# Kernel optimization log

Measured on AMD Instinct MI355X. Metric: run time of the kernel, lower is better.

Reference implementation:

```python
import jax, jax.numpy as jnp
import numpy as np

S = 16          # slice count (init kwarg)
EPS = 1e-5      # BN2d default eps


def markov_sub(m, s):
    """Vectorized get_markov_sub. m: [C, C] -> [s, C, C].
    ms[i][a,b] = where(m[i,b] > 0, m[a,b], 0); mss[k] = max over rows i in slice k.
    Equivalent closed form via per-column any/all positivity of the slice rows."""
    C = m.shape[0]
    pos = (m > 0.0).reshape(s, C // s, C)          # [s, slice_size, C]
    any_p = pos.any(axis=1)[:, None, :]            # [s, 1, C]
    all_p = pos.all(axis=1)[:, None, :]            # [s, 1, C]
    mb = m[None, :, :]                             # [1, C, C]
    return jnp.where(all_p, mb,
                     jnp.where(any_p, jnp.maximum(mb, 0.0), jnp.zeros_like(mb)))


def setup_inputs() -> dict:
    key = jax.random.key(0)
    ks = jax.random.split(key, 8)
    N, C, H, W = 4, 256, 32, 32
    s = S
    feats = jax.random.normal(ks[0], (N, C, H, W), jnp.float32)
    adj_matrix = jax.random.normal(ks[1], (N, C, C), jnp.float32)
    # three 1x1 conv layers: in = S*C, out = C (stacked on leading axis)
    conv_w = jax.random.normal(ks[2], (3, C, s * C), jnp.float32) / np.sqrt(s * C).astype(np.float32)
    conv_b = jax.random.normal(ks[3], (3, C), jnp.float32) * 0.01
    bn_gamma = jnp.ones((3, C), jnp.float32)
    bn_beta = jnp.zeros((3, C), jnp.float32)
    bn_mean = jax.random.normal(ks[4], (3, C), jnp.float32) * 0.1
    bn_var = jax.random.uniform(ks[5], (3, C), jnp.float32, minval=0.5, maxval=1.5)
    return {"feats": feats, "adj_matrix": adj_matrix, "conv_w": conv_w,
            "conv_b": conv_b, "bn_gamma": bn_gamma, "bn_beta": bn_beta,
            "bn_mean": bn_mean, "bn_var": bn_var}


def reference(feats, adj_matrix, conv_w, conv_b, bn_gamma, bn_beta, bn_mean, bn_var):
    N, C, H, W = feats.shape
    s = S
    # per-sample markov sub-adjacencies, computed once and reused across layers
    mss = jax.vmap(lambda m: markov_sub(m, s))(adj_matrix)      # [N, S, C, C]
    mss = mss.reshape(N, s * C, C)                              # [N, S*C, C]
    outs = []
    x = feats
    for l in range(3):
        xp = x.reshape(N, C, H * W)                             # [N, C, HW]
        y = jnp.einsum('nkc,ncp->nkp', mss, xp)                 # sparse.mm -> [N, S*C, HW]
        y = jnp.einsum('ok,nkp->nop', conv_w[l], y) + conv_b[l][None, :, None]
        scale = (bn_gamma[l] * jax.lax.rsqrt(bn_var[l] + EPS))[None, :, None]
        y = (y - bn_mean[l][None, :, None]) * scale + bn_beta[l][None, :, None]
        y = jax.nn.relu(y).reshape(N, C, H, W)
        outs.append(y)
        x = y
    return tuple(outs)
```

## Files before the change

kernel.cpp:

```cpp
#include <hip/hip_runtime.h>
#include <stdint.h>

#define CC   256
#define SSL  16
#define NB   4
#define HWP  1024
#define K1   4096
#define EPSV 1e-5f

typedef __attribute__((ext_vector_type(8))) short bf16x8;
typedef __attribute__((ext_vector_type(4))) float f32x4;

__device__ __forceinline__ ushort f2bf(float f) {
    uint32_t u = __float_as_uint(f);
    uint32_t r = (u + 0x7FFFu + ((u >> 16) & 1u)) >> 16;
    return (ushort)r;
}

__global__ __launch_bounds__(256) void flags_kernel(const float* __restrict__ adj,
                                                    uint8_t* __restrict__ flags) {
    const int nk = blockIdx.x;
    const int n = nk >> 4, k = nk & 15;
    const int b = threadIdx.x;
    const float* m = adj + (size_t)n * CC * CC;
    bool allp = true, anyp = false;
#pragma unroll
    for (int i = 0; i < 16; ++i) {
        float v = m[(size_t)(k * 16 + i) * CC + b];
        bool p = v > 0.0f;
        allp = allp && p;
        anyp = anyp || p;
    }
    flags[(size_t)nk * CC + b] = allp ? (uint8_t)2 : (anyp ? (uint8_t)1 : (uint8_t)0);
}

__global__ __launch_bounds__(256) void convw_bf16_kernel(const float* __restrict__ w,
                                                         ushort* __restrict__ wb) {
    const int idx = (blockIdx.x * 256 + threadIdx.x) * 4;
    float4 v = *(const float4*)(w + idx);
    ushort4 o = {f2bf(v.x), f2bf(v.y), f2bf(v.z), f2bf(v.w)};
    *(ushort4*)(wb + idx) = o;
}

__global__ __launch_bounds__(256) void msst_kernel(const float* __restrict__ adj,
                                                   const uint8_t* __restrict__ flags,
                                                   ushort* __restrict__ msst) {
    const int n = blockIdx.y;
    const int at = blockIdx.x >> 2, bt = blockIdx.x & 3;
    const int a0 = at * 64, b0 = bt * 64;
    const float* m = adj + (size_t)n * CC * CC;
    __shared__ float Ms[64][68];
    __shared__ uint8_t Fl[16][64];
    const int t = threadIdx.x;
    {
        const int ar = t >> 2, bq = (t & 3) * 16;
        const float* src = m + (size_t)(a0 + ar) * CC + b0 + bq;
#pragma unroll
        for (int i = 0; i < 4; ++i)
            *(float4*)&Ms[ar][bq + i * 4] = *(const float4*)(src + i * 4);
        const int k = t >> 4, b4 = (t & 15) * 4;
        *(uchar4*)&Fl[k][b4] = *(const uchar4*)(flags + (size_t)(n * SSL + k) * CC + b0 + b4);
    }
    __syncthreads();
    const int bl = t >> 2, ac = (t & 3) * 16;
    ushort bx[16], bp[16];
#pragma unroll
    for (int i = 0; i < 16; ++i) {
        float x = Ms[ac + i][bl];
        bx[i] = f2bf(x);
        bp[i] = f2bf(fmaxf(x, 0.0f));
    }
    ushort* dst = msst + ((size_t)(n * CC + b0 + bl)) * K1 + a0 + ac;
#pragma unroll
    for (int k = 0; k < 16; ++k) {
        const uint8_t f = Fl[k][bl];
        ushort* dk = dst + k * CC;
#pragma unroll
        for (int a4 = 0; a4 < 4; ++a4) {
            ushort4 o;
            o.x = (f == 2) ? bx[a4 * 4 + 0] : ((f == 1) ? bp[a4 * 4 + 0] : (ushort)0);
            o.y = (f == 2) ? bx[a4 * 4 + 1] : ((f == 1) ? bp[a4 * 4 + 1] : (ushort)0);
            o.z = (f == 2) ? bx[a4 * 4 + 2] : ((f == 1) ? bp[a4 * 4 + 2] : (ushort)0);
            o.w = (f == 2) ? bx[a4 * 4 + 3] : ((f == 1) ? bp[a4 * 4 + 3] : (ushort)0);
            *(ushort4*)(dk + a4 * 4) = o;
        }
    }
}

__global__ __launch_bounds__(256) void featsT_kernel(const float* __restrict__ feats,
                                                     ushort* __restrict__ fT) {
    const int n = blockIdx.y;
    const int ct = blockIdx.x >> 4, pt = blockIdx.x & 15;
    const int c0 = ct * 64, p0 = pt * 64;
    const float* src = feats + ((size_t)n * CC + c0) * HWP + p0;
    __shared__ float Ts[64][68];
    const int t = threadIdx.x;
    const int cr = t >> 2, pq = (t & 3) * 16;
#pragma unroll
    for (int i = 0; i < 4; ++i)
        *(float4*)&Ts[cr][pq + i * 4] = *(const float4*)(src + (size_t)cr * HWP + pq + i * 4);
    __syncthreads();
    const int pl = t >> 2, cc0 = (t & 3) * 16;
    ushort* dst = fT + ((size_t)n * HWP + p0 + pl) * CC + c0 + cc0;
#pragma unroll
    for (int a4 = 0; a4 < 4; ++a4) {
        ushort4 o;
        o.x = f2bf(Ts[cc0 + a4 * 4 + 0][pl]);
        o.y = f2bf(Ts[cc0 + a4 * 4 + 1][pl]);
        o.z = f2bf(Ts[cc0 + a4 * 4 + 2][pl]);
        o.w = f2bf(Ts[cc0 + a4 * 4 + 3][pl]);
        *(ushort4*)(dst + a4 * 4) = o;
    }
}

__global__ __launch_bounds__(256) void weff_mfma(const ushort* __restrict__ Aw,
                                                 const ushort* __restrict__ Bm,
                                                 float* __restrict__ wpart) {
    const int tile = blockIdx.x;
    const int ln = blockIdx.y;
    const int sp = blockIdx.z;
    const int l = ln >> 2, n = ln & 3;
    const int trow = (tile >> 1) * 128, tcol = (tile & 1) * 128;
    const ushort* A = Aw + (size_t)l * CC * K1;
    const ushort* B = Bm + (size_t)n * CC * K1;
    __shared__ ushort Al[128][40];
    __shared__ ushort Bl[128][40];
    const int t = threadIdx.x;
    const int wv = t >> 6, L = t & 63;
    const int wr = (wv >> 1) * 64, wc = (wv & 1) * 64;
    const int l16 = L & 15, q = L >> 4;
    const int r0 = t >> 2, kq0 = (t & 3) * 8;
    f32x4 acc[4][4];
#pragma unroll
    for (int i = 0; i < 4; ++i)
#pragma unroll
        for (int j = 0; j < 4; ++j)
            acc[i][j] = (f32x4){0.f, 0.f, 0.f, 0.f};

    const int kbase = sp * 512;
    for (int kt = 0; kt < 16; ++kt) {
        const int kk = kbase + kt * 32;
        int4 a0 = *(const int4*)(A + (size_t)(trow + r0) * K1 + kk + kq0);
        int4 a1 = *(const int4*)(A + (size_t)(trow + 64 + r0) * K1 + kk + kq0);
        int4 b0 = *(const int4*)(B + (size_t)(tcol + r0) * K1 + kk + kq0);
        int4 b1 = *(const int4*)(B + (size_t)(tcol + 64 + r0) * K1 + kk + kq0);
        __syncthreads();
        *(int4*)&Al[r0][kq0] = a0;
        *(int4*)&Al[64 + r0][kq0] = a1;
        *(int4*)&Bl[r0][kq0] = b0;
        *(int4*)&Bl[64 + r0][kq0] = b1;
        __syncthreads();
        bf16x8 af[4], bfr[4];
#pragma unroll
        for (int i = 0; i < 4; ++i)
            af[i] = *(const bf16x8*)&Al[wr + i * 16 + l16][q * 8];
#pragma unroll
        for (int j = 0; j < 4; ++j)
            bfr[j] = *(const bf16x8*)&Bl[wc + j * 16 + l16][q * 8];
#pragma unroll
        for (int i = 0; i < 4; ++i)
#pragma unroll
            for (int j = 0; j < 4; ++j)
                acc[i][j] = __builtin_amdgcn_mfma_f32_16x16x32_bf16(af[i], bfr[j], acc[i][j], 0, 0, 0);
    }

    float* W = wpart + ((size_t)sp * 12 + ln) * (CC * CC);
#pragma unroll
    for (int i = 0; i < 4; ++i)
#pragma unroll
        for (int j = 0; j < 4; ++j) {
            const int o = trow + wr + i * 16 + q * 4;
            const int b = tcol + wc + j * 16 + l16;
#pragma unroll
            for (int r = 0; r < 4; ++r)
                W[(size_t)(o + r) * CC + b] = acc[i][j][r];
        }
}

__global__ __launch_bounds__(256) void reduce_kernel(const float* __restrict__ wpart,
                                                     const float* __restrict__ gamma,
                                                     const float* __restrict__ var,
                                                     ushort* __restrict__ Ws) {
    const int idx = (blockIdx.x * 256 + threadIdx.x) * 4;
    const int ln = idx >> 16;
    const int l = ln >> 2;
    const int o = (idx >> 8) & 255;
    float4 s = {0.f, 0.f, 0.f, 0.f};
#pragma unroll
    for (int sp = 0; sp < 8; ++sp) {
        float4 v = *(const float4*)(wpart + (size_t)sp * 12 * 65536 + idx);
        s.x += v.x; s.y += v.y; s.z += v.z; s.w += v.w;
    }
    const float sc = gamma[l * CC + o] * rsqrtf(var[l * CC + o] + EPSV);
    ushort4 ob = {f2bf(s.x * sc), f2bf(s.y * sc), f2bf(s.z * sc), f2bf(s.w * sc)};
    *(ushort4*)(Ws + idx) = ob;
}

__global__ __launch_bounds__(256) void layer_mfma(const ushort* __restrict__ xT,
                                                  const ushort* __restrict__ Wsl,
                                                  const float* __restrict__ convb_l,
                                                  const float* __restrict__ gamma_l,
                                                  const float* __restrict__ beta_l,
                                                  const float* __restrict__ mean_l,
                                                  const float* __restrict__ var_l,
                                                  float* __restrict__ outl,
                                                  ushort* __restrict__ xTn) {
    const int n = blockIdx.y;
    const int pt = blockIdx.x & 15, ot = blockIdx.x >> 4;
    const ushort* Axt = xT + (size_t)n * HWP * CC + (size_t)pt * 64 * CC;
    const ushort* Bw  = Wsl + (size_t)n * CC * CC + (size_t)ot * 64 * CC;
    __shared__ ushort Al[64][40];
    __shared__ ushort Bl[64][40];
    const int t = threadIdx.x;
    const int wv = t >> 6, L = t & 63;
    const int wr = (wv >> 1) * 32, wc = (wv & 1) * 32;
    const int l16 = L & 15, q = L >> 4;
    const int r0 = t >> 2, kq0 = (t & 3) * 8;
    f32x4 acc[2][2];
#pragma unroll
    for (int i = 0; i < 2; ++i)
#pragma unroll
        for (int j = 0; j < 2; ++j)
            acc[i][j] = (f32x4){0.f, 0.f, 0.f, 0.f};

    for (int kt = 0; kt < 8; ++kt) {
        const int kk = kt * 32;
        int4 av = *(const int4*)(Axt + (size_t)r0 * CC + kk + kq0);
        int4 bv = *(const int4*)(Bw + (size_t)r0 * CC + kk + kq0);
        __syncthreads();
        *(int4*)&Al[r0][kq0] = av;
        *(int4*)&Bl[r0][kq0] = bv;
        __syncthreads();
        bf16x8 af[2], bfr[2];
#pragma unroll
        for (int i = 0; i < 2; ++i)
            af[i] = *(const bf16x8*)&Al[wr + i * 16 + l16][q * 8];
#pragma unroll
        for (int j = 0; j < 2; ++j)
            bfr[j] = *(const bf16x8*)&Bl[wc + j * 16 + l16][q * 8];
#pragma unroll
        for (int i = 0; i < 2; ++i)
#pragma unroll
            for (int j = 0; j < 2; ++j)
                acc[i][j] = __builtin_amdgcn_mfma_f32_16x16x32_bf16(af[i], bfr[j], acc[i][j], 0, 0, 0);
    }

    float* outn = outl + (size_t)n * CC * HWP;
    ushort* xtn = xTn + (size_t)n * HWP * CC;
#pragma unroll
    for (int i = 0; i < 2; ++i)
#pragma unroll
        for (int j = 0; j < 2; ++j) {
            const int p = pt * 64 + wr + i * 16 + q * 4;
            const int o = ot * 64 + wc + j * 16 + l16;
            const float sc = gamma_l[o] * rsqrtf(var_l[o] + EPSV);
            const float b2 = sc * (convb_l[o] - mean_l[o]) + beta_l[o];
            float v0 = fmaxf(acc[i][j][0] + b2, 0.f);
            float v1 = fmaxf(acc[i][j][1] + b2, 0.f);
            float v2 = fmaxf(acc[i][j][2] + b2, 0.f);
            float v3 = fmaxf(acc[i][j][3] + b2, 0.f);
            *(float4*)(outn + (size_t)o * HWP + p) = (float4){v0, v1, v2, v3};
            xtn[(size_t)(p + 0) * CC + o] = f2bf(v0);
            xtn[(size_t)(p + 1) * CC + o] = f2bf(v1);
            xtn[(size_t)(p + 2) * CC + o] = f2bf(v2);
            xtn[(size_t)(p + 3) * CC + o] = f2bf(v3);
        }
}

extern "C" void kernel_launch(void* const* d_in, const int* in_sizes, int n_in,
                              void* d_out, int out_size, void* d_ws, size_t ws_size,
                              hipStream_t stream) {
    const float* feats  = (const float*)d_in[0];
    const float* adj    = (const float*)d_in[1];
    const float* conv_w = (const float*)d_in[2];
    const float* conv_b = (const float*)d_in[3];
    const float* gamma  = (const float*)d_in[4];
    const float* beta   = (const float*)d_in[5];
    const float* mean   = (const float*)d_in[6];
    const float* var    = (const float*)d_in[7];
    float* out = (float*)d_out;

    char* ws = (char*)d_ws;
    uint8_t* flags  = (uint8_t*)ws;
    ushort*  convwb = (ushort*)(ws + 65536);
    ushort*  msst   = (ushort*)(ws + 65536 + 6291456);
    ushort*  Wsb    = (ushort*)(ws + 65536 + 6291456 + 8388608);
    ushort*  fT0    = (ushort*)(ws + 65536 + 6291456 + 8388608 + 1572864);
    float*   wpart  = (float*)(ws + 65536 + 6291456 + 8388608 + 1572864 + 2097152);
    ushort*  xT1    = (ushort*)wpart;
    ushort*  xT2    = xT1 + (size_t)NB * HWP * CC;
    ushort*  xT3    = xT2 + (size_t)NB * HWP * CC;

    flags_kernel<<<NB * SSL, CC, 0, stream>>>(adj, flags);
    convw_bf16_kernel<<<3072, 256, 0, stream>>>(conv_w, convwb);
    msst_kernel<<<dim3(16, NB), 256, 0, stream>>>(adj, flags, msst);
    featsT_kernel<<<dim3(64, NB), 256, 0, stream>>>(feats, fT0);
    weff_mfma<<<dim3(4, 12, 8), 256, 0, stream>>>(convwb, msst, wpart);
    reduce_kernel<<<768, 256, 0, stream>>>(wpart, gamma, var, Wsb);

    const ushort* xin[3] = {fT0, xT1, xT2};
    ushort* xout[3] = {xT1, xT2, xT3};
    for (int l = 0; l < 3; ++l) {
        layer_mfma<<<dim3(64, NB), 256, 0, stream>>>(
            xin[l], Wsb + (size_t)l * NB * CC * CC,
            conv_b + l * CC, gamma + l * CC, beta + l * CC, mean + l * CC, var + l * CC,
            out + (size_t)l * NB * CC * HWP, xout[l]);
    }
}
```

Baseline: 131.4 us.

## Merge prep kernels and coalesce epilogue stores via shared-memory transposes

Folds the flags, conv-weight bf16 conversion and feature transpose kernels into one launch, cutting launch count. The weff partial-product store is transposed to float4 writes, and the reduce kernel now transposes back through shared memory so Ws keeps its original layout. The layer epilogue stages the activated tile in shared memory so both the fp32 output and the bf16 transposed activation are written with vectorized, coalesced stores instead of scattered 2-byte writes. This adds shared memory and a barrier per layer block.

Measured after the change: 136.9 us. +4.2%, slower.

```diff
diff --git a/kernel.cpp b/kernel.cpp
--- a/kernel.cpp
+++ b/kernel.cpp
@@ -17,29 +17,58 @@
     return (ushort)r;
 }
 
-__global__ __launch_bounds__(256) void flags_kernel(const float* __restrict__ adj,
-                                                    uint8_t* __restrict__ flags) {
-    const int nk = blockIdx.x;
-    const int n = nk >> 4, k = nk & 15;
-    const int b = threadIdx.x;
-    const float* m = adj + (size_t)n * CC * CC;
-    bool allp = true, anyp = false;
-#pragma unroll
-    for (int i = 0; i < 16; ++i) {
-        float v = m[(size_t)(k * 16 + i) * CC + b];
-        bool p = v > 0.0f;
-        allp = allp && p;
-        anyp = anyp || p;
-    }
-    flags[(size_t)nk * CC + b] = allp ? (uint8_t)2 : (anyp ? (uint8_t)1 : (uint8_t)0);
-}
-
-__global__ __launch_bounds__(256) void convw_bf16_kernel(const float* __restrict__ w,
-                                                         ushort* __restrict__ wb) {
-    const int idx = (blockIdx.x * 256 + threadIdx.x) * 4;
-    float4 v = *(const float4*)(w + idx);
-    ushort4 o = {f2bf(v.x), f2bf(v.y), f2bf(v.z), f2bf(v.w)};
-    *(ushort4*)(wb + idx) = o;
+__global__ __launch_bounds__(256) void prep1_kernel(const float* __restrict__ adj,
+                                                    const float* __restrict__ feats,
+                                                    const float* __restrict__ conv_w,
+                                                    uint8_t* __restrict__ flags,
+                                                    ushort* __restrict__ fT,
+                                                    ushort* __restrict__ wb) {
+    __shared__ float Ts[64][68];
+    const int bid = blockIdx.x;
+    const int t = threadIdx.x;
+    if (bid < 64) {
+        const int n = bid >> 4, k = bid & 15;
+        const float* m = adj + (size_t)n * CC * CC;
+        bool allp = true, anyp = false;
+#pragma unroll
+        for (int i = 0; i < 16; ++i) {
+            float v = m[(size_t)(k * 16 + i) * CC + t];
+            bool p = v > 0.0f;
+            allp = allp && p;
+            anyp = anyp || p;
+        }
+        flags[(size_t)bid * CC + t] = allp ? (uint8_t)2 : (anyp ? (uint8_t)1 : (uint8_t)0);
+    } else if (bid < 320) {
+        const int f = bid - 64;
+        const int n = f >> 6, r = f & 63;
+        const int c0 = (r >> 4) * 64, p0 = (r & 15) * 64;
+        const float* src = feats + ((size_t)n * CC + c0) * HWP + p0;
+        const int cr = t >> 2, pq = (t & 3) * 16;
+#pragma unroll
+        for (int i = 0; i < 4; ++i)
+            *(float4*)&Ts[cr][pq + i * 4] = *(const float4*)(src + (size_t)cr * HWP + pq + i * 4);
+        __syncthreads();
+        const int pl = t >> 2, cc0 = (t & 3) * 16;
+        ushort* dst = fT + ((size_t)n * HWP + p0 + pl) * CC + c0 + cc0;
+#pragma unroll
+        for (int a4 = 0; a4 < 4; ++a4) {
+            ushort4 o;
+            o.x = f2bf(Ts[cc0 + a4 * 4 + 0][pl]);
+            o.y = f2bf(Ts[cc0 + a4 * 4 + 1][pl]);
+            o.z = f2bf(Ts[cc0 + a4 * 4 + 2][pl]);
+            o.w = f2bf(Ts[cc0 + a4 * 4 + 3][pl]);
+            *(ushort4*)(dst + a4 * 4) = o;
+        }
+    } else {
+        const int c = bid - 320;
+        const int idx = (c * 256 + t) * 16;
+#pragma unroll
+        for (int i = 0; i < 4; ++i) {
+            float4 v = *(const float4*)(conv_w + idx + i * 4);
+            ushort4 o = {f2bf(v.x), f2bf(v.y), f2bf(v.z), f2bf(v.w)};
+            *(ushort4*)(wb + idx + i * 4) = o;
+        }
+    }
 }
 
 __global__ __launch_bounds__(256) void msst_kernel(const float* __restrict__ adj,
@@ -84,32 +113,6 @@
             o.w = (f == 2) ? bx[a4 * 4 + 3] : ((f == 1) ? bp[a4 * 4 + 3] : (ushort)0);
             *(ushort4*)(dk + a4 * 4) = o;
         }
-    }
-}
-
-__global__ __launch_bounds__(256) void featsT_kernel(const float* __restrict__ feats,
-                                                     ushort* __restrict__ fT) {
-    const int n = blockIdx.y;
-    const int ct = blockIdx.x >> 4, pt = blockIdx.x & 15;
-    const int c0 = ct * 64, p0 = pt * 64;
-    const float* src = feats + ((size_t)n * CC + c0) * HWP + p0;
-    __shared__ float Ts[64][68];
-    const int t = threadIdx.x;
-    const int cr = t >> 2, pq = (t & 3) * 16;
-#pragma unroll
-    for (int i = 0; i < 4; ++i)
-        *(float4*)&Ts[cr][pq + i * 4] = *(const float4*)(src + (size_t)cr * HWP + pq + i * 4);
-    __syncthreads();
-    const int pl = t >> 2, cc0 = (t & 3) * 16;
-    ushort* dst = fT + ((size_t)n * HWP + p0 + pl) * CC + c0 + cc0;
-#pragma unroll
-    for (int a4 = 0; a4 < 4; ++a4) {
-        ushort4 o;
-        o.x = f2bf(Ts[cc0 + a4 * 4 + 0][pl]);
-        o.y = f2bf(Ts[cc0 + a4 * 4 + 1][pl]);
-        o.z = f2bf(Ts[cc0 + a4 * 4 + 2][pl]);
-        o.w = f2bf(Ts[cc0 + a4 * 4 + 3][pl]);
-        *(ushort4*)(dst + a4 * 4) = o;
     }
 }
 
@@ -169,11 +172,10 @@
     for (int i = 0; i < 4; ++i)
 #pragma unroll
         for (int j = 0; j < 4; ++j) {
-            const int o = trow + wr + i * 16 + q * 4;
-            const int b = tcol + wc + j * 16 + l16;
-#pragma unroll
-            for (int r = 0; r < 4; ++r)
-                W[(size_t)(o + r) * CC + b] = acc[i][j][r];
+            const int ob = trow + wr + i * 16 + q * 4;
+            const int b  = tcol + wc + j * 16 + l16;
+            *(float4*)(W + (size_t)b * CC + ob) =
+                (float4){acc[i][j][0], acc[i][j][1], acc[i][j][2], acc[i][j][3]};
         }
 }
 
@@ -181,19 +183,42 @@
                                                      const float* __restrict__ gamma,
                                                      const float* __restrict__ var,
                                                      ushort* __restrict__ Ws) {
-    const int idx = (blockIdx.x * 256 + threadIdx.x) * 4;
-    const int ln = idx >> 16;
+    const int ln = blockIdx.y;
     const int l = ln >> 2;
-    const int o = (idx >> 8) & 255;
-    float4 s = {0.f, 0.f, 0.f, 0.f};
+    const int bt = blockIdx.x >> 2, ot = blockIdx.x & 3;
+    __shared__ ushort T[64][72];
+    __shared__ float scv[64];
+    const int t = threadIdx.x;
+    if (t < 64) {
+        const int o = ot * 64 + t;
+        scv[t] = gamma[l * CC + o] * rsqrtf(var[l * CC + o] + EPSV);
+    }
+    __syncthreads();
+    const int bl = t >> 2, oc = (t & 3) * 16;
+    const float* base = wpart + (size_t)ln * (CC * CC) + (size_t)(bt * 64 + bl) * CC + ot * 64 + oc;
+    float s[16] = {};
 #pragma unroll
     for (int sp = 0; sp < 8; ++sp) {
-        float4 v = *(const float4*)(wpart + (size_t)sp * 12 * 65536 + idx);
-        s.x += v.x; s.y += v.y; s.z += v.z; s.w += v.w;
-    }
-    const float sc = gamma[l * CC + o] * rsqrtf(var[l * CC + o] + EPSV);
-    ushort4 ob = {f2bf(s.x * sc), f2bf(s.y * sc), f2bf(s.z * sc), f2bf(s.w * sc)};
-    *(ushort4*)(Ws + idx) = ob;
+        const float* p = base + (size_t)sp * 12 * CC * CC;
+#pragma unroll
+        for (int c = 0; c < 4; ++c) {
+            float4 v = *(const float4*)(p + c * 4);
+            s[c * 4 + 0] += v.x; s[c * 4 + 1] += v.y;
+            s[c * 4 + 2] += v.z; s[c * 4 + 3] += v.w;
+        }
+    }
+#pragma unroll
+    for (int e = 0; e < 16; ++e)
+        T[oc + e][bl] = f2bf(s[e] * scv[oc + e]);
+    __syncthreads();
+    const int ol = t >> 2, b0 = (t & 3) * 16;
+    ushort* dst = Ws + ((size_t)ln * CC + ot * 64 + ol) * CC + bt * 64 + b0;
+#pragma unroll
+    for (int c = 0; c < 4; ++c) {
+        ushort4 o = {T[ol][b0 + c * 4 + 0], T[ol][b0 + c * 4 + 1],
+                     T[ol][b0 + c * 4 + 2], T[ol][b0 + c * 4 + 3]};
+        *(ushort4*)(dst + c * 4) = o;
+    }
 }
 
 __global__ __launch_bounds__(256) void layer_mfma(const ushort* __restrict__ xT,
@@ -211,6 +236,7 @@
     const ushort* Bw  = Wsl + (size_t)n * CC * CC + (size_t)ot * 64 * CC;
     __shared__ ushort Al[64][40];
     __shared__ ushort Bl[64][40];
+    __shared__ float S[64][68];
     const int t = threadIdx.x;
     const int wv = t >> 6, L = t & 63;
     const int wr = (wv >> 1) * 32, wc = (wv & 1) * 32;
@@ -245,26 +271,45 @@
                 acc[i][j] = __builtin_amdgcn_mfma_f32_16x16x32_bf16(af[i], bfr[j], acc[i][j], 0, 0, 0);
     }
 
+#pragma unroll
+    for (int j = 0; j < 2; ++j) {
+        const int ol = wc + j * 16 + l16;
+        const int og = ot * 64 + ol;
+        const float sc = gamma_l[og] * rsqrtf(var_l[og] + EPSV);
+        const float b2 = sc * (convb_l[og] - mean_l[og]) + beta_l[og];
+#pragma unroll
+        for (int i = 0; i < 2; ++i) {
+            const int pl = wr + i * 16 + q * 4;
+            S[pl + 0][ol] = fmaxf(acc[i][j][0] + b2, 0.f);
+            S[pl + 1][ol] = fmaxf(acc[i][j][1] + b2, 0.f);
+            S[pl + 2][ol] = fmaxf(acc[i][j][2] + b2, 0.f);
+            S[pl + 3][ol] = fmaxf(acc[i][j][3] + b2, 0.f);
+        }
+    }
+    __syncthreads();
+
     float* outn = outl + (size_t)n * CC * HWP;
     ushort* xtn = xTn + (size_t)n * HWP * CC;
-#pragma unroll
-    for (int i = 0; i < 2; ++i)
-#pragma unroll
-        for (int j = 0; j < 2; ++j) {
-            const int p = pt * 64 + wr + i * 16 + q * 4;
-            const int o = ot * 64 + wc + j * 16 + l16;
-            const float sc = gamma_l[o] * rsqrtf(var_l[o] + EPSV);
-            const float b2 = sc * (convb_l[o] - mean_l[o]) + beta_l[o];
-            float v0 = fmaxf(acc[i][j][0] + b2, 0.f);
-            float v1 = fmaxf(acc[i][j][1] + b2, 0.f);
-            float v2 = fmaxf(acc[i][j][2] + b2, 0.f);
-            float v3 = fmaxf(acc[i][j][3] + b2, 0.f);
-            *(float4*)(outn + (size_t)o * HWP + p) = (float4){v0, v1, v2, v3};
-            xtn[(size_t)(p + 0) * CC + o] = f2bf(v0);
-            xtn[(size_t)(p + 1) * CC + o] = f2bf(v1);
-            xtn[(size_t)(p + 2) * CC + o] = f2bf(v2);
-            xtn[(size_t)(p + 3) * CC + o] = f2bf(v3);
-        }
+    {
+        const int ol = t >> 2, p0 = (t & 3) * 16;
+        float* op = outn + (size_t)(ot * 64 + ol) * HWP + pt * 64 + p0;
+#pragma unroll
+        for (int c = 0; c < 4; ++c) {
+            float4 v = {S[p0 + c * 4 + 0][ol], S[p0 + c * 4 + 1][ol],
+                        S[p0 + c * 4 + 2][ol], S[p0 + c * 4 + 3][ol]};
+            *(float4*)(op + c * 4) = v;
+        }
+    }
+    {
+        const int pl = t >> 2, c0 = (t & 3) * 16;
+        ushort* xp = xtn + (size_t)(pt * 64 + pl) * CC + ot * 64 + c0;
+#pragma unroll
+        for (int c = 0; c < 4; ++c) {
+            ushort4 o = {f2bf(S[pl][c0 + c * 4 + 0]), f2bf(S[pl][c0 + c * 4 + 1]),
+                         f2bf(S[pl][c0 + c * 4 + 2]), f2bf(S[pl][c0 + c * 4 + 3])};
+            *(ushort4*)(xp + c * 4) = o;
+        }
+    }
 }
 
 extern "C" void kernel_launch(void* const* d_in, const int* in_sizes, int n_in,
@@ -291,12 +336,10 @@
     ushort*  xT2    = xT1 + (size_t)NB * HWP * CC;
     ushort*  xT3    = xT2 + (size_t)NB * HWP * CC;
 
-    flags_kernel<<<NB * SSL, CC, 0, stream>>>(adj, flags);
-    convw_bf16_kernel<<<3072, 256, 0, stream>>>(conv_w, convwb);
+    prep1_kernel<<<1088, 256, 0, stream>>>(adj, feats, conv_w, flags, fT0, convwb);
     msst_kernel<<<dim3(16, NB), 256, 0, stream>>>(adj, flags, msst);
-    featsT_kernel<<<dim3(64, NB), 256, 0, stream>>>(feats, fT0);
     weff_mfma<<<dim3(4, 12, 8), 256, 0, stream>>>(convwb, msst, wpart);
-    reduce_kernel<<<768, 256, 0, stream>>>(wpart, gamma, var, Wsb);
+    reduce_kernel<<<dim3(16, 12), 256, 0, stream>>>(wpart, gamma, var, Wsb);
 
     const ushort* xin[3] = {fT0, xT1, xT2};
     ushort* xout[3] = {xT1, xT2, xT3};
```

## Fuse prep kernels, drop split-K reduction in weff GEMM, prefetch loads

Applied to the files above, without the earlier changes.

Merges the flags, conv weight cast, msst build and feature transpose into one heterogeneous prep kernel, so only one launch is needed and the flags are computed in shared memory. The weff GEMM now uses 64x64 tiles over the full K range and applies the BN scale directly, removing the split-K partial buffer and the separate reduce kernel. Register prefetch of the next K tile is added to both GEMMs. The last layer also skips writing its unused transposed bf16 copy. The cost is a long serial K loop of 64 iterations per weff block on fewer, smaller tiles, and a launch that leaves a quarter of the weff blocks idle.

Result: slower. 144.9 us (+10.2%).

```diff
diff --git a/kernel.cpp b/kernel.cpp
--- a/kernel.cpp
+++ b/kernel.cpp
@@ -17,183 +17,177 @@
     return (ushort)r;
 }
 
-__global__ __launch_bounds__(256) void flags_kernel(const float* __restrict__ adj,
-                                                    uint8_t* __restrict__ flags) {
-    const int nk = blockIdx.x;
-    const int n = nk >> 4, k = nk & 15;
-    const int b = threadIdx.x;
-    const float* m = adj + (size_t)n * CC * CC;
-    bool allp = true, anyp = false;
-#pragma unroll
-    for (int i = 0; i < 16; ++i) {
-        float v = m[(size_t)(k * 16 + i) * CC + b];
-        bool p = v > 0.0f;
-        allp = allp && p;
-        anyp = anyp || p;
-    }
-    flags[(size_t)nk * CC + b] = allp ? (uint8_t)2 : (anyp ? (uint8_t)1 : (uint8_t)0);
-}
-
-__global__ __launch_bounds__(256) void convw_bf16_kernel(const float* __restrict__ w,
-                                                         ushort* __restrict__ wb) {
-    const int idx = (blockIdx.x * 256 + threadIdx.x) * 4;
-    float4 v = *(const float4*)(w + idx);
-    ushort4 o = {f2bf(v.x), f2bf(v.y), f2bf(v.z), f2bf(v.w)};
-    *(ushort4*)(wb + idx) = o;
-}
-
-__global__ __launch_bounds__(256) void msst_kernel(const float* __restrict__ adj,
-                                                   const uint8_t* __restrict__ flags,
+__global__ __launch_bounds__(256) void prep_kernel(const float* __restrict__ adj,
+                                                   const float* __restrict__ feats,
+                                                   const float* __restrict__ conv_w,
+                                                   ushort* __restrict__ fT,
+                                                   ushort* __restrict__ wb,
                                                    ushort* __restrict__ msst) {
-    const int n = blockIdx.y;
-    const int at = blockIdx.x >> 2, bt = blockIdx.x & 3;
-    const int a0 = at * 64, b0 = bt * 64;
-    const float* m = adj + (size_t)n * CC * CC;
-    __shared__ float Ms[64][68];
-    __shared__ uint8_t Fl[16][64];
+    __shared__ char smem[67584];
+    const int bid = blockIdx.x;
     const int t = threadIdx.x;
-    {
-        const int ar = t >> 2, bq = (t & 3) * 16;
-        const float* src = m + (size_t)(a0 + ar) * CC + b0 + bq;
+    if (bid < 256) {
+        float (*Ts)[68] = (float(*)[68])smem;
+        const int n = bid >> 6, r = bid & 63;
+        const int c0 = (r >> 4) * 64, p0 = (r & 15) * 64;
+        const float* src = feats + ((size_t)n * CC + c0) * HWP + p0;
+        const int cr = t >> 2, pq = (t & 3) * 16;
 #pragma unroll
         for (int i = 0; i < 4; ++i)
-            *(float4*)&Ms[ar][bq + i * 4] = *(const float4*)(src + i * 4);
-        const int k = t >> 4, b4 = (t & 15) * 4;
-        *(uchar4*)&Fl[k][b4] = *(const uchar4*)(flags + (size_t)(n * SSL + k) * CC + b0 + b4);
-    }
-    __syncthreads();
-    const int bl = t >> 2, ac = (t & 3) * 16;
-    ushort bx[16], bp[16];
-#pragma unroll
-    for (int i = 0; i < 16; ++i) {
-        float x = Ms[ac + i][bl];
-        bx[i] = f2bf(x);
-        bp[i] = f2bf(fmaxf(x, 0.0f));
-    }
-    ushort* dst = msst + ((size_t)(n * CC + b0 + bl)) * K1 + a0 + ac;
-#pragma unroll
-    for (int k = 0; k < 16; ++k) {
-        const uint8_t f = Fl[k][bl];
-        ushort* dk = dst + k * CC;
+            *(float4*)&Ts[cr][pq + i * 4] = *(const float4*)(src + (size_t)cr * HWP + pq + i * 4);
+        __syncthreads();
+        const int pl = t >> 2, cc0 = (t & 3) * 16;
+        ushort* dst = fT + ((size_t)n * HWP + p0 + pl) * CC + c0 + cc0;
 #pragma unroll
         for (int a4 = 0; a4 < 4; ++a4) {
             ushort4 o;
-            o.x = (f == 2) ? bx[a4 * 4 + 0] : ((f == 1) ? bp[a4 * 4 + 0] : (ushort)0);
-            o.y = (f == 2) ? bx[a4 * 4 + 1] : ((f == 1) ? bp[a4 * 4 + 1] : (ushort)0);
-            o.z = (f == 2) ? bx[a4 * 4 + 2] : ((f == 1) ? bp[a4 * 4 + 2] : (ushort)0);
-            o.w = (f == 2) ? bx[a4 * 4 + 3] : ((f == 1) ? bp[a4 * 4 + 3] : (ushort)0);
-            *(ushort4*)(dk + a4 * 4) = o;
-        }
-    }
-}
-
-__global__ __launch_bounds__(256) void featsT_kernel(const float* __restrict__ feats,
-                                                     ushort* __restrict__ fT) {
-    const int n = blockIdx.y;
-    const int ct = blockIdx.x >> 4, pt = blockIdx.x & 15;
-    const int c0 = ct * 64, p0 = pt * 64;
-    const float* src = feats + ((size_t)n * CC + c0) * HWP + p0;
-    __shared__ float Ts[64][68];
-    const int t = threadIdx.x;
-    const int cr = t >> 2, pq = (t & 3) * 16;
-#pragma unroll
-    for (int i = 0; i < 4; ++i)
-        *(float4*)&Ts[cr][pq + i * 4] = *(const float4*)(src + (size_t)cr * HWP + pq + i * 4);
-    __syncthreads();
-    const int pl = t >> 2, cc0 = (t & 3) * 16;
-    ushort* dst = fT + ((size_t)n * HWP + p0 + pl) * CC + c0 + cc0;
-#pragma unroll
-    for (int a4 = 0; a4 < 4; ++a4) {
-        ushort4 o;
-        o.x = f2bf(Ts[cc0 + a4 * 4 + 0][pl]);
-        o.y = f2bf(Ts[cc0 + a4 * 4 + 1][pl]);
-        o.z = f2bf(Ts[cc0 + a4 * 4 + 2][pl]);
-        o.w = f2bf(Ts[cc0 + a4 * 4 + 3][pl]);
-        *(ushort4*)(dst + a4 * 4) = o;
+            o.x = f2bf(Ts[cc0 + a4 * 4 + 0][pl]);
+            o.y = f2bf(Ts[cc0 + a4 * 4 + 1][pl]);
+            o.z = f2bf(Ts[cc0 + a4 * 4 + 2][pl]);
+            o.w = f2bf(Ts[cc0 + a4 * 4 + 3][pl]);
+            *(ushort4*)(dst + a4 * 4) = o;
+        }
+    } else if (bid < 1024) {
+        const int c = bid - 256;
+        const int idx = (c * 256 + t) * 16;
+#pragma unroll
+        for (int i = 0; i < 4; ++i) {
+            float4 v = *(const float4*)(conv_w + idx + i * 4);
+            ushort4 o = {f2bf(v.x), f2bf(v.y), f2bf(v.z), f2bf(v.w)};
+            *(ushort4*)(wb + idx + i * 4) = o;
+        }
+    } else {
+        float (*Mc)[65] = (float(*)[65])smem;
+        uint8_t* fl = (uint8_t*)(smem + 66560);
+        const int q = bid - 1024;
+        const int n = q >> 4, at = (q >> 2) & 3, bt = q & 3;
+        const float* m = adj + (size_t)n * CC * CC + bt * 64;
+#pragma unroll
+        for (int it = 0; it < 16; ++it) {
+            const int r = it * 16 + (t >> 4), c = (t & 15) * 4;
+            *(float4*)&Mc[r][c] = *(const float4*)(m + (size_t)r * CC + c);
+        }
+        __syncthreads();
+#pragma unroll
+        for (int e = 0; e < 4; ++e) {
+            const int pair = t + e * 256;
+            const int k = pair >> 6, b = pair & 63;
+            bool allp = true, anyp = false;
+#pragma unroll
+            for (int i = 0; i < 16; ++i) {
+                const bool p = Mc[k * 16 + i][b] > 0.0f;
+                allp = allp && p;
+                anyp = anyp || p;
+            }
+            fl[k * 64 + b] = allp ? (uint8_t)2 : (anyp ? (uint8_t)1 : (uint8_t)0);
+        }
+        __syncthreads();
+        const int b = t >> 2, a0 = at * 64 + (t & 3) * 16;
+        ushort bx[16], bp[16];
+#pragma unroll
+        for (int e = 0; e < 16; ++e) {
+            const float x = Mc[a0 + e][b];
+            bx[e] = f2bf(x);
+            bp[e] = f2bf(fmaxf(x, 0.0f));
+        }
+        ushort* dst = msst + ((size_t)(n * CC + bt * 64 + b)) * K1 + a0;
+#pragma unroll
+        for (int k = 0; k < 16; ++k) {
+            const uint8_t f = fl[k * 64 + b];
+            ushort* dk = dst + k * CC;
+#pragma unroll
+            for (int a4 = 0; a4 < 4; ++a4) {
+                ushort4 o;
+                o.x = (f == 2) ? bx[a4 * 4 + 0] : ((f == 1) ? bp[a4 * 4 + 0] : (ushort)0);
+                o.y = (f == 2) ? bx[a4 * 4 + 1] : ((f == 1) ? bp[a4 * 4 + 1] : (ushort)0);
+                o.z = (f == 2) ? bx[a4 * 4 + 2] : ((f == 1) ? bp[a4 * 4 + 2] : (ushort)0);
+                o.w = (f == 2) ? bx[a4 * 4 + 3] : ((f == 1) ? bp[a4 * 4 + 3] : (ushort)0);
+                *(ushort4*)(dk + a4 * 4) = o;
+            }
+        }
     }
 }
 
 __global__ __launch_bounds__(256) void weff_mfma(const ushort* __restrict__ Aw,
                                                  const ushort* __restrict__ Bm,
-                                                 float* __restrict__ wpart) {
-    const int tile = blockIdx.x;
-    const int ln = blockIdx.y;
-    const int sp = blockIdx.z;
-    const int l = ln >> 2, n = ln & 3;
-    const int trow = (tile >> 1) * 128, tcol = (tile & 1) * 128;
+                                                 const float* __restrict__ gamma,
+                                                 const float* __restrict__ var,
+                                                 ushort* __restrict__ Ws) {
+    const int x = blockIdx.x;
+    const int g = x & 15;
+    if (g >= 12) return;
+    const int mI = x >> 4;
+    const int l = g >> 2, ot = g & 3;
+    const int n = mI >> 2, bt = mI & 3;
+    const int ln = l * 4 + n;
+    const int o0 = ot * 64, b0 = bt * 64;
     const ushort* A = Aw + (size_t)l * CC * K1;
     const ushort* B = Bm + (size_t)n * CC * K1;
-    __shared__ ushort Al[128][40];
-    __shared__ ushort Bl[128][40];
+    __shared__ ushort Al[64][72];
+    __shared__ ushort Bl[64][72];
     const int t = threadIdx.x;
     const int wv = t >> 6, L = t & 63;
-    const int wr = (wv >> 1) * 64, wc = (wv & 1) * 64;
+    const int wr = (wv >> 1) * 32, wc = (wv & 1) * 32;
     const int l16 = L & 15, q = L >> 4;
-    const int r0 = t >> 2, kq0 = (t & 3) * 8;
-    f32x4 acc[4][4];
-#pragma unroll
-    for (int i = 0; i < 4; ++i)
-#pragma unroll
-        for (int j = 0; j < 4; ++j)
+    const int r0 = t >> 2, kq0 = (t & 3) * 16;
+    f32x4 acc[2][2];
+#pragma unroll
+    for (int i = 0; i < 2; ++i)
+#pragma unroll
+        for (int j = 0; j < 2; ++j)
             acc[i][j] = (f32x4){0.f, 0.f, 0.f, 0.f};
 
-    const int kbase = sp * 512;
-    for (int kt = 0; kt < 16; ++kt) {
-        const int kk = kbase + kt * 32;
-        int4 a0 = *(const int4*)(A + (size_t)(trow + r0) * K1 + kk + kq0);
-        int4 a1 = *(const int4*)(A + (size_t)(trow + 64 + r0) * K1 + kk + kq0);
-        int4 b0 = *(const int4*)(B + (size_t)(tcol + r0) * K1 + kk + kq0);
-        int4 b1 = *(const int4*)(B + (size_t)(tcol + 64 + r0) * K1 + kk + kq0);
-        __syncthreads();
-        *(int4*)&Al[r0][kq0] = a0;
-        *(int4*)&Al[64 + r0][kq0] = a1;
-        *(int4*)&Bl[r0][kq0] = b0;
-        *(int4*)&Bl[64 + r0][kq0] = b1;
-        __syncthreads();
-        bf16x8 af[4], bfr[4];
-#pragma unroll
-        for (int i = 0; i < 4; ++i)
-            af[i] = *(const bf16x8*)&Al[wr + i * 16 + l16][q * 8];
-#pragma unroll
-        for (int j = 0; j < 4; ++j)
-            bfr[j] = *(const bf16x8*)&Bl[wc + j * 16 + l16][q * 8];
-#pragma unroll
-        for (int i = 0; i < 4; ++i)
-#pragma unroll
-            for (int j = 0; j < 4; ++j)
-                acc[i][j] = __builtin_amdgcn_mfma_f32_16x16x32_bf16(af[i], bfr[j], acc[i][j], 0, 0, 0);
+    const ushort* Ap = A + (size_t)(o0 + r0) * K1 + kq0;
+    const ushort* Bp = B + (size_t)(b0 + r0) * K1 + kq0;
+    int4 a0v = *(const int4*)(Ap);
+    int4 a1v = *(const int4*)(Ap + 8);
+    int4 b0v = *(const int4*)(Bp);
+    int4 b1v = *(const int4*)(Bp + 8);
+
+    for (int kt = 0; kt < 64; ++kt) {
+        __syncthreads();
+        *(int4*)&Al[r0][kq0] = a0v;
+        *(int4*)&Al[r0][kq0 + 8] = a1v;
+        *(int4*)&Bl[r0][kq0] = b0v;
+        *(int4*)&Bl[r0][kq0 + 8] = b1v;
+        __syncthreads();
+        if (kt < 63) {
+            const int kk = (kt + 1) * 64;
+            a0v = *(const int4*)(Ap + kk);
+            a1v = *(const int4*)(Ap + kk + 8);
+            b0v = *(const int4*)(Bp + kk);
+            b1v = *(const int4*)(Bp + kk + 8);
+        }
+#pragma unroll
+        for (int ks = 0; ks < 2; ++ks) {
+            bf16x8 af[2], bfr[2];
+#pragma unroll
+            for (int i = 0; i < 2; ++i)
+                af[i] = *(const bf16x8*)&Al[wr + i * 16 + l16][ks * 32 + q * 8];
+#pragma unroll
+            for (int j = 0; j < 2; ++j)
+                bfr[j] = *(const bf16x8*)&Bl[wc + j * 16 + l16][ks * 32 + q * 8];
+#pragma unroll
+            for (int i = 0; i < 2; ++i)
+#pragma unroll
+                for (int j = 0; j < 2; ++j)
+                    acc[i][j] = __builtin_amdgcn_mfma_f32_16x16x32_bf16(af[i], bfr[j], acc[i][j], 0, 0, 0);
+        }
     }
 
-    float* W = wpart + ((size_t)sp * 12 + ln) * (CC * CC);
-#pragma unroll
-    for (int i = 0; i < 4; ++i)
-#pragma unroll
-        for (int j = 0; j < 4; ++j) {
-            const int o = trow + wr + i * 16 + q * 4;
-            const int b = tcol + wc + j * 16 + l16;
-#pragma unroll
-            for (int r = 0; r < 4; ++r)
-                W[(size_t)(o + r) * CC + b] = acc[i][j][r];
-        }
-}
-
-__global__ __launch_bounds__(256) void reduce_kernel(const float* __restrict__ wpart,
-                                                     const float* __restrict__ gamma,
-                                                     const float* __restrict__ var,
-                                                     ushort* __restrict__ Ws) {
-    const int idx = (blockIdx.x * 256 + threadIdx.x) * 4;
-    const int ln = idx >> 16;
-    const int l = ln >> 2;
-    const int o = (idx >> 8) & 255;
-    float4 s = {0.f, 0.f, 0.f, 0.f};
-#pragma unroll
-    for (int sp = 0; sp < 8; ++sp) {
-        float4 v = *(const float4*)(wpart + (size_t)sp * 12 * 65536 + idx);
-        s.x += v.x; s.y += v.y; s.z += v.z; s.w += v.w;
-    }
-    const float sc = gamma[l * CC + o] * rsqrtf(var[l * CC + o] + EPSV);
-    ushort4 ob = {f2bf(s.x * sc), f2bf(s.y * sc), f2bf(s.z * sc), f2bf(s.w * sc)};
-    *(ushort4*)(Ws + idx) = ob;
+#pragma unroll
+    for (int i = 0; i < 2; ++i)
+#pragma unroll
+        for (int j = 0; j < 2; ++j) {
+            const int ob = o0 + wr + i * 16 + q * 4;
+            const int b = b0 + wc + j * 16 + l16;
+#pragma unroll
+            for (int r = 0; r < 4; ++r) {
+                const int o = ob + r;
+                const float sc = gamma[l * CC + o] * rsqrtf(var[l * CC + o] + EPSV);
+                Ws[((size_t)ln * CC + o) * CC + b] = f2bf(acc[i][j][r] * sc);
+            }
+        }
 }
 
 __global__ __launch_bounds__(256) void layer_mfma(const ushort* __restrict__ xT,
@@ -223,14 +217,18 @@
         for (int j = 0; j < 2; ++j)
             acc[i][j] = (f32x4){0.f, 0.f, 0.f, 0.f};
 
+    int4 av = *(const int4*)(Axt + (size_t)r0 * CC + kq0);
+    int4 bv = *(const int4*)(Bw + (size_t)r0 * CC + kq0);
     for (int kt = 0; kt < 8; ++kt) {
-        const int kk = kt * 32;
-        int4 av = *(const int4*)(Axt + (size_t)r0 * CC + kk + kq0);
-        int4 bv = *(const int4*)(Bw + (size_t)r0 * CC + kk + kq0);
         __syncthreads();
         *(int4*)&Al[r0][kq0] = av;
         *(int4*)&Bl[r0][kq0] = bv;
         __syncthreads();
+        if (kt < 7) {
+            const int kk = (kt + 1) * 32;
+            av = *(const int4*)(Axt + (size_t)r0 * CC + kk + kq0);
+            bv = *(const int4*)(Bw + (size_t)r0 * CC + kk + kq0);
+        }
         bf16x8 af[2], bfr[2];
 #pragma unroll
         for (int i = 0; i < 2; ++i)
@@ -246,7 +244,7 @@
     }
 
     float* outn = outl + (size_t)n * CC * HWP;
-    ushort* xtn = xTn + (size_t)n * HWP * CC;
+    ushort* xtn = xTn ? xTn + (size_t)n * HWP * CC : (ushort*)0;
 #pragma unroll
     for (int i = 0; i < 2; ++i)
 #pragma unroll
@@ -260,10 +258,12 @@
             float v2 = fmaxf(acc[i][j][2] + b2, 0.f);
             float v3 = fmaxf(acc[i][j][3] + b2, 0.f);
             *(float4*)(outn + (size_t)o * HWP + p) = (float4){v0, v1, v2, v3};
-            xtn[(size_t)(p + 0) * CC + o] = f2bf(v0);
-            xtn[(size_t)(p + 1) * CC + o] = f2bf(v1);
-            xtn[(size_t)(p + 2) * CC + o] = f2bf(v2);
-            xtn[(size_t)(p + 3) * CC + o] = f2bf(v3);
+            if (xtn) {
+                xtn[(size_t)(p + 0) * CC + o] = f2bf(v0);
+                xtn[(size_t)(p + 1) * CC + o] = f2bf(v1);
+                xtn[(size_t)(p + 2) * CC + o] = f2bf(v2);
+                xtn[(size_t)(p + 3) * CC + o] = f2bf(v3);
+            }
         }
 }
 
@@ -281,25 +281,18 @@
     float* out = (float*)d_out;
 
     char* ws = (char*)d_ws;
-    uint8_t* flags  = (uint8_t*)ws;
-    ushort*  convwb = (ushort*)(ws + 65536);
-    ushort*  msst   = (ushort*)(ws + 65536 + 6291456);
-    ushort*  Wsb    = (ushort*)(ws + 65536 + 6291456 + 8388608);
-    ushort*  fT0    = (ushort*)(ws + 65536 + 6291456 + 8388608 + 1572864);
-    float*   wpart  = (float*)(ws + 65536 + 6291456 + 8388608 + 1572864 + 2097152);
-    ushort*  xT1    = (ushort*)wpart;
-    ushort*  xT2    = xT1 + (size_t)NB * HWP * CC;
-    ushort*  xT3    = xT2 + (size_t)NB * HWP * CC;
-
-    flags_kernel<<<NB * SSL, CC, 0, stream>>>(adj, flags);
-    convw_bf16_kernel<<<3072, 256, 0, stream>>>(conv_w, convwb);
-    msst_kernel<<<dim3(16, NB), 256, 0, stream>>>(adj, flags, msst);
-    featsT_kernel<<<dim3(64, NB), 256, 0, stream>>>(feats, fT0);
-    weff_mfma<<<dim3(4, 12, 8), 256, 0, stream>>>(convwb, msst, wpart);
-    reduce_kernel<<<768, 256, 0, stream>>>(wpart, gamma, var, Wsb);
+    ushort* convwb = (ushort*)ws;
+    ushort* msst   = (ushort*)(ws + 6291456);
+    ushort* Wsb    = (ushort*)(ws + 6291456 + 8388608);
+    ushort* fT0    = (ushort*)(ws + 6291456 + 8388608 + 1572864);
+    ushort* xT1    = (ushort*)(ws + 6291456 + 8388608 + 1572864 + 2097152);
+    ushort* xT2    = (ushort*)(ws + 6291456 + 8388608 + 1572864 + 2097152 + 2097152);
+
+    prep_kernel<<<1088, 256, 0, stream>>>(adj, feats, conv_w, fT0, convwb, msst);
+    weff_mfma<<<256, 256, 0, stream>>>(convwb, msst, gamma, var, Wsb);
 
     const ushort* xin[3] = {fT0, xT1, xT2};
-    ushort* xout[3] = {xT1, xT2, xT3};
+    ushort* xout[3] = {xT1, xT2, (ushort*)0};
     for (int l = 0; l < 3; ++l) {
         layer_mfma<<<dim3(64, NB), 256, 0, stream>>>(
             xin[l], Wsb + (size_t)l * NB * CC * CC,
```

## Halve layer GEMM tile rows, double grid, and prefetch next K slice into registers

Applied to the files above, without the earlier changes.

The per-layer MFMA kernel now uses 32x64 output tiles instead of 64x64, doubling the grid from 256 to 512 blocks per layer so more CUs are busy. Global loads for the next K slice are issued before the current slice's MFMAs (register double-buffering) to overlap load latency with compute. A null check makes the transposed bf16 output optional, though the last layer still passes a buffer. The cost is less data reuse per block and twice as many B-tile loads.

Result: no change. 131.6 us (+0.1%).

```diff
diff --git a/kernel.cpp b/kernel.cpp
--- a/kernel.cpp
+++ b/kernel.cpp
@@ -206,65 +206,60 @@
                                                   float* __restrict__ outl,
                                                   ushort* __restrict__ xTn) {
     const int n = blockIdx.y;
-    const int pt = blockIdx.x & 15, ot = blockIdx.x >> 4;
-    const ushort* Axt = xT + (size_t)n * HWP * CC + (size_t)pt * 64 * CC;
+    const int pt = blockIdx.x & 31, ot = blockIdx.x >> 5;
+    const ushort* Axt = xT + (size_t)n * HWP * CC + (size_t)pt * 32 * CC;
     const ushort* Bw  = Wsl + (size_t)n * CC * CC + (size_t)ot * 64 * CC;
-    __shared__ ushort Al[64][40];
+    __shared__ ushort Al[32][40];
     __shared__ ushort Bl[64][40];
     const int t = threadIdx.x;
     const int wv = t >> 6, L = t & 63;
-    const int wr = (wv >> 1) * 32, wc = (wv & 1) * 32;
+    const int wr = (wv >> 1) * 16, wc = (wv & 1) * 32;
     const int l16 = L & 15, q = L >> 4;
-    const int r0 = t >> 2, kq0 = (t & 3) * 8;
-    f32x4 acc[2][2];
-#pragma unroll
-    for (int i = 0; i < 2; ++i)
-#pragma unroll
-        for (int j = 0; j < 2; ++j)
-            acc[i][j] = (f32x4){0.f, 0.f, 0.f, 0.f};
-
+    const int ra = t >> 3, ka0 = (t & 7) * 4;
+    const int rb = t >> 2, kb0 = (t & 3) * 8;
+    f32x4 acc[2];
+    acc[0] = (f32x4){0.f, 0.f, 0.f, 0.f};
+    acc[1] = (f32x4){0.f, 0.f, 0.f, 0.f};
+
+    int2 av = *(const int2*)(Axt + (size_t)ra * CC + ka0);
+    int4 bv = *(const int4*)(Bw + (size_t)rb * CC + kb0);
     for (int kt = 0; kt < 8; ++kt) {
-        const int kk = kt * 32;
-        int4 av = *(const int4*)(Axt + (size_t)r0 * CC + kk + kq0);
-        int4 bv = *(const int4*)(Bw + (size_t)r0 * CC + kk + kq0);
         __syncthreads();
-        *(int4*)&Al[r0][kq0] = av;
-        *(int4*)&Bl[r0][kq0] = bv;
+        *(int2*)&Al[ra][ka0] = av;
+        *(int4*)&Bl[rb][kb0] = bv;
         __syncthreads();
-        bf16x8 af[2], bfr[2];
-#pragma unroll
-        for (int i = 0; i < 2; ++i)
-            af[i] = *(const bf16x8*)&Al[wr + i * 16 + l16][q * 8];
-#pragma unroll
-        for (int j = 0; j < 2; ++j)
-            bfr[j] = *(const bf16x8*)&Bl[wc + j * 16 + l16][q * 8];
-#pragma unroll
-        for (int i = 0; i < 2; ++i)
-#pragma unroll
-            for (int j = 0; j < 2; ++j)
-                acc[i][j] = __builtin_amdgcn_mfma_f32_16x16x32_bf16(af[i], bfr[j], acc[i][j], 0, 0, 0);
+        if (kt < 7) {
+            const int kk = (kt + 1) * 32;
+            av = *(const int2*)(Axt + (size_t)ra * CC + kk + ka0);
+            bv = *(const int4*)(Bw + (size_t)rb * CC + kk + kb0);
+        }
+        bf16x8 af = *(const bf16x8*)&Al[wr + l16][q * 8];
+        bf16x8 b0 = *(const bf16x8*)&Bl[wc + l16][q * 8];
+        bf16x8 b1 = *(const bf16x8*)&Bl[wc + 16 + l16][q * 8];
+        acc[0] = __builtin_amdgcn_mfma_f32_16x16x32_bf16(af, b0, acc[0], 0, 0, 0);
+        acc[1] = __builtin_amdgcn_mfma_f32_16x16x32_bf16(af, b1, acc[1], 0, 0, 0);
     }
 
     float* outn = outl + (size_t)n * CC * HWP;
-    ushort* xtn = xTn + (size_t)n * HWP * CC;
-#pragma unroll
-    for (int i = 0; i < 2; ++i)
-#pragma unroll
-        for (int j = 0; j < 2; ++j) {
-            const int p = pt * 64 + wr + i * 16 + q * 4;
-            const int o = ot * 64 + wc + j * 16 + l16;
-            const float sc = gamma_l[o] * rsqrtf(var_l[o] + EPSV);
-            const float b2 = sc * (convb_l[o] - mean_l[o]) + beta_l[o];
-            float v0 = fmaxf(acc[i][j][0] + b2, 0.f);
-            float v1 = fmaxf(acc[i][j][1] + b2, 0.f);
-            float v2 = fmaxf(acc[i][j][2] + b2, 0.f);
-            float v3 = fmaxf(acc[i][j][3] + b2, 0.f);
-            *(float4*)(outn + (size_t)o * HWP + p) = (float4){v0, v1, v2, v3};
+    ushort* xtn = xTn ? xTn + (size_t)n * HWP * CC : (ushort*)0;
+#pragma unroll
+    for (int j = 0; j < 2; ++j) {
+        const int p = pt * 32 + wr + q * 4;
+        const int o = ot * 64 + wc + j * 16 + l16;
+        const float sc = gamma_l[o] * rsqrtf(var_l[o] + EPSV);
+        const float b2 = sc * (convb_l[o] - mean_l[o]) + beta_l[o];
+        float v0 = fmaxf(acc[j][0] + b2, 0.f);
+        float v1 = fmaxf(acc[j][1] + b2, 0.f);
+        float v2 = fmaxf(acc[j][2] + b2, 0.f);
+        float v3 = fmaxf(acc[j][3] + b2, 0.f);
+        *(float4*)(outn + (size_t)o * HWP + p) = (float4){v0, v1, v2, v3};
+        if (xtn) {
             xtn[(size_t)(p + 0) * CC + o] = f2bf(v0);
             xtn[(size_t)(p + 1) * CC + o] = f2bf(v1);
             xtn[(size_t)(p + 2) * CC + o] = f2bf(v2);
             xtn[(size_t)(p + 3) * CC + o] = f2bf(v3);
         }
+    }
 }
 
 extern "C" void kernel_launch(void* const* d_in, const int* in_sizes, int n_in,
@@ -301,7 +296,7 @@
     const ushort* xin[3] = {fT0, xT1, xT2};
     ushort* xout[3] = {xT1, xT2, xT3};
     for (int l = 0; l < 3; ++l) {
-        layer_mfma<<<dim3(64, NB), 256, 0, stream>>>(
+        layer_mfma<<<dim3(128, NB), 256, 0, stream>>>(
             xin[l], Wsb + (size_t)l * NB * CC * CC,
             conv_b + l * CC, gamma + l * CC, beta + l * CC, mean + l * CC, var + l * CC,
             out + (size_t)l * NB * CC * HWP, xout[l]);
```
